# Optimization experiments

Hardware: AMD Instinct MI355X
Metric: run time of the kernel (lower is better)

## Reference

```python
import jax, jax.numpy as jnp
import numpy as np

N = 50000        # nodes
E = 800000       # edges (before self-loops)
IN = 128         # in_dim
H = 2            # heads
C1 = 64          # hidden_dim (per head)
D1 = H * C1      # conv1 concat output = 128
OUT = 64         # out_dim
C2 = 2 * OUT     # conv2 per-head channels = 128 (concat=False -> mean over heads)
NEG = 0.2        # GATv2 leaky_relu negative slope
EPS = 1e-5       # BatchNorm eps


def setup_inputs() -> dict:
    key = jax.random.key(0)
    ks = jax.random.split(key, 14)
    s = 0.05
    inp = {
        "x": jax.random.normal(ks[0], (N, IN), jnp.float32),
        "edge_index": jax.random.randint(ks[1], (2, E), 0, N, dtype=jnp.int32),
        # conv1 (GATv2: lin_l for source, lin_r for target, att vector per head)
        "W_l1": jax.random.normal(ks[2], (IN, D1), jnp.float32) * s,
        "b_l1": jnp.zeros((D1,), jnp.float32),
        "W_r1": jax.random.normal(ks[3], (IN, D1), jnp.float32) * s,
        "b_r1": jnp.zeros((D1,), jnp.float32),
        "att1": jax.random.normal(ks[4], (H, C1), jnp.float32) * s,
        "bias1": jnp.zeros((D1,), jnp.float32),
        # batch_norm1 (affine)
        "gamma1": jnp.ones((D1,), jnp.float32),
        "beta1": jnp.zeros((D1,), jnp.float32),
        # conv2
        "W_l2": jax.random.normal(ks[5], (D1, H * C2), jnp.float32) * s,
        "b_l2": jnp.zeros((H * C2,), jnp.float32),
        "W_r2": jax.random.normal(ks[6], (D1, H * C2), jnp.float32) * s,
        "b_r2": jnp.zeros((H * C2,), jnp.float32),
        "att2": jax.random.normal(ks[7], (H, C2), jnp.float32) * s,
        "bias2": jnp.zeros((C2,), jnp.float32),
    }
    return inp


def gatv2_layer(x, src, dst, W_l, b_l, W_r, b_r, att, bias, concat):
    Hh, Cc = att.shape
    x_l = (x @ W_l + b_l).reshape(N, Hh, Cc)   # source transform
    x_r = (x @ W_r + b_r).reshape(N, Hh, Cc)   # target transform
    # per-edge GATv2 score: att . leaky_relu(x_l[j] + x_r[i])
    e = jax.nn.leaky_relu(x_l[src] + x_r[dst], NEG)      # [E', H, C]
    logit = jnp.einsum("ehc,hc->eh", e, att)              # [E', H]
    # segment softmax over incoming edges of each target node
    m = jax.ops.segment_max(logit, dst, num_segments=N)   # [N, H]
    ex = jnp.exp(logit - m[dst])
    den = jax.ops.segment_sum(ex, dst, num_segments=N)    # [N, H]
    alpha = ex / den[dst]                                  # [E', H]
    out = jax.ops.segment_sum(x_l[src] * alpha[:, :, None], dst, num_segments=N)
    out = out.reshape(N, Hh * Cc) if concat else out.mean(axis=1)
    return out + bias


def batchnorm(x, gamma=None, beta=None):
    mu = x.mean(axis=0)
    var = x.var(axis=0)  # biased variance, as used by BN for normalization
    xn = (x - mu) * jax.lax.rsqrt(var + EPS)
    if gamma is not None:
        xn = xn * gamma + beta
    return xn


def reference(x, edge_index, W_l1, b_l1, W_r1, b_r1, att1, bias1, gamma1, beta1,
              W_l2, b_l2, W_r2, b_r2, att2, bias2):
    loops = jnp.arange(N, dtype=edge_index.dtype)
    src = jnp.concatenate([edge_index[0], loops])  # add self-loops (PyG default)
    dst = jnp.concatenate([edge_index[1], loops])
    h = gatv2_layer(x, src, dst, W_l1, b_l1, W_r1, b_r1, att1, bias1, True)
    h = jax.nn.relu(batchnorm(h, gamma1, beta1))
    o = gatv2_layer(h, src, dst, W_l2, b_l2, W_r2, b_r2, att2, bias2, False)
    mu_part = batchnorm(o[:, :OUT])                      # affine=False
    return jnp.concatenate([mu_part, jax.nn.softplus(o[:, OUT:])], axis=1)
```

## Files before the change

### kernel.cpp

```cpp
#include <hip/hip_runtime.h>
#include <hip/hip_bf16.h>
#include <math.h>

#define NNODES 50000
#define NEDGES 800000
#define EPTOT  (NEDGES + NNODES)
#define NEG_SLOPE 0.2f
#define BN_EPS 1e-5f
#define LOG2E 1.44269504088896f
#define ESLOT 64

#define PB_SC  3321
#define PB_W1  (PB_SC + 128)
#define PB_W2  (PB_W1 + 256)

typedef __hip_bfloat16 bf16;
typedef __attribute__((ext_vector_type(8))) short short8;
typedef __attribute__((ext_vector_type(4))) float f32x4;
typedef __attribute__((ext_vector_type(2))) float f32x2;

__device__ __forceinline__ unsigned short f2us(float f){
    return (unsigned short)(__bfloat16_as_ushort(__float2bfloat16(f)));
}
__device__ __forceinline__ f32x2 unpk(unsigned int w){
    union { unsigned int u; float f; } lo, hi;
    lo.u = w << 16; hi.u = w & 0xffff0000u;
    f32x2 r; r.x = lo.f; r.y = hi.f; return r;
}
__device__ __forceinline__ f32x2 pkmax(f32x2 a, f32x2 b){
#if __has_builtin(__builtin_elementwise_max)
    return __builtin_elementwise_max(a, b);
#else
    f32x2 r; r.x = fmaxf(a.x, b.x); r.y = fmaxf(a.y, b.y); return r;
#endif
}
__device__ __forceinline__ unsigned int pack2(float a, float b){
    return (unsigned int)f2us(a) | ((unsigned int)f2us(b) << 16);
}


__global__ __launch_bounds__(256) void misc_prep(
    const int* __restrict__ ei, int* __restrict__ cnt, int* __restrict__ esrc,
    const float* __restrict__ Wl1, const float* __restrict__ Wr1,
    const float* __restrict__ bl1, const float* __restrict__ br1,
    bf16* __restrict__ WT1, float* __restrict__ bc1,
    const float* __restrict__ Wl2, const float* __restrict__ Wr2,
    const float* __restrict__ bl2, const float* __restrict__ br2,
    bf16* __restrict__ WT2, float* __restrict__ bc2)
{
    int b = blockIdx.x;
    if (b < PB_SC){
        int e = b * 256 + threadIdx.x;
        if (e < EPTOT){
            int s, d;
            if (e < NEDGES){ s = ei[e]; d = ei[NEDGES + e]; } else { s = d = e - NEDGES; }
            int pos = atomicAdd(&cnt[d], 1);
            if (pos < ESLOT) esrc[(d << 6) + pos] = s;
        }
    } else if (b < PB_W1){
        int i = (b - PB_SC) * 256 + threadIdx.x;
        int r = i >> 7, k = i & 127;
        const float* W = (r < 128) ? Wl1 : Wr1;
        int c = (r < 128) ? r : r - 128;
        WT1[i] = __float2bfloat16(W[k * 128 + c]);
        if (k == 0) bc1[r] = (r < 128) ? bl1[c] : br1[c];
    } else {
        int i = (b - PB_W1) * 256 + threadIdx.x;
        int r = i >> 7, k = i & 127;
        const float* W = (r < 256) ? Wl2 : Wr2;
        int c = (r < 256) ? r : r - 256;
        WT2[i] = __float2bfloat16(W[k * 256 + c]);
        if (k == 0) bc2[r] = (r < 256) ? bl2[c] : br2[c];
    }
}


template<int DTOT, bool F32A>
__global__ __launch_bounds__(128) void mfma_gemm(
    const void* __restrict__ A, const bf16* __restrict__ WT,
    const float* __restrict__ biascat,
    bf16* __restrict__ xl, bf16* __restrict__ xr)
{
    constexpr int TILES = DTOT / 64;
    int wave = threadIdx.x >> 6;
    int lane = threadIdx.x & 63;
    int quad = lane >> 4;
    int l16  = lane & 15;
    int m0 = blockIdx.x * 128 + wave * 64;
    const short* Ap = (const short*)A;
    const float* Af = (const float*)A;
    const short* Bp = (const short*)WT;

    short8 af[4][4];
    #pragma unroll
    for (int k = 0; k < 4; ++k)
        #pragma unroll
        for (int mt = 0; mt < 4; ++mt){
            int m = m0 + mt * 16 + l16;
            m = (m < NNODES) ? m : (NNODES - 1);
            if (F32A){
                float4 v0 = *(const float4*)(Af + (size_t)m * 128 + k * 32 + quad * 8);
                float4 v1 = *(const float4*)(Af + (size_t)m * 128 + k * 32 + quad * 8 + 4);
                unsigned int* u = (unsigned int*)&af[k][mt];
                u[0] = pack2(v0.x, v0.y); u[1] = pack2(v0.z, v0.w);
                u[2] = pack2(v1.x, v1.y); u[3] = pack2(v1.z, v1.w);
            } else {
                af[k][mt] = *(const short8*)(Ap + (size_t)m * 128 + k * 32 + quad * 8);
            }
        }

    for (int t = 0; t < TILES; ++t){
        int n0 = (blockIdx.y * TILES + t) * 64;
        f32x4 acc[4][4] = {};
        #pragma unroll
        for (int k = 0; k < 4; ++k){
            short8 bfr[4];
            #pragma unroll
            for (int nt = 0; nt < 4; ++nt){
                int n = n0 + nt * 16 + l16;
                bfr[nt] = *(const short8*)(Bp + (size_t)n * 128 + k * 32 + quad * 8);
            }
            #pragma unroll
            for (int mt = 0; mt < 4; ++mt)
                #pragma unroll
                for (int nt = 0; nt < 4; ++nt)
                    acc[mt][nt] = __builtin_amdgcn_mfma_f32_16x16x32_bf16(af[k][mt], bfr[nt], acc[mt][nt], 0, 0, 0);
        }
        #pragma unroll
        for (int nt = 0; nt < 4; ++nt){
            int n = n0 + nt * 16 + l16;
            float bi = biascat[n];
            bf16* outp = (n < DTOT) ? xl : xr;
            int c = (n < DTOT) ? n : n - DTOT;
            #pragma unroll
            for (int mt = 0; mt < 4; ++mt)
                #pragma unroll
                for (int r = 0; r < 4; ++r){
                    int m = m0 + mt * 16 + quad * 4 + r;
                    if (m < NNODES)
                        outp[(size_t)m * DTOT + c] = __float2bfloat16(acc[mt][nt][r] + bi);
                }
        }
    }
}


template<int C, bool MEAN>
__global__ __launch_bounds__(128) void gat_aggregate(
    const bf16* __restrict__ xl, const bf16* __restrict__ xr,
    const float* __restrict__ att, const int* __restrict__ cnt,
    const int* __restrict__ esrc, void* __restrict__ outv,
    const float* __restrict__ bias2)
{
    constexpr int G  = C / 8;
    constexpr int E  = 64 / G;
    constexpr int HC = 2 * C;
    __shared__ float tmp[HC];
    int n    = blockIdx.x;
    int lane = threadIdx.x & 63;
    int head = threadIdx.x >> 6;
    int g    = lane / G;
    int cl   = lane % G;
    int rowoff = head * (C * 2) + cl * 16;
    const char* xlb = (const char*)xl;

    uint4 xw = *(const uint4*)((const char*)xr + (size_t)n * (HC * 2) + rowoff);
    f32x2 xr0 = unpk(xw.x), xr1 = unpk(xw.y), xr2v = unpk(xw.z), xr3 = unpk(xw.w);
    const float* ap = att + head * C + cl * 8;
    f32x2 av0 = {ap[0] * LOG2E, ap[1] * LOG2E};
    f32x2 av1 = {ap[2] * LOG2E, ap[3] * LOG2E};
    f32x2 av2 = {ap[4] * LOG2E, ap[5] * LOG2E};
    f32x2 av3 = {ap[6] * LOG2E, ap[7] * LOG2E};

    int e0 = n << 6;
    int e1 = e0 + cnt[n];

    float den = 0.f;
    f32x2 a0 = {0.f,0.f}, a1 = {0.f,0.f}, a2 = {0.f,0.f}, a3 = {0.f,0.f};
    for (int p0 = e0; p0 < e1; p0 += 2 * E){
        int pa = p0 + g;
        int pb = p0 + E + g;
        float mka = (pa < e1) ? 0.f : -1e30f;
        float mkb = (pb < e1) ? 0.f : -1e30f;
        int sa = esrc[(pa < e1) ? pa : (e1 - 1)];
        int sb = esrc[(pb < e1) ? pb : (e1 - 1)];
        uint4 wa = *(const uint4*)(xlb + (size_t)sa * (HC * 2) + rowoff);
        uint4 wb = *(const uint4*)(xlb + (size_t)sb * (HC * 2) + rowoff);

        f32x2 xa0 = unpk(wa.x), xa1 = unpk(wa.y), xa2 = unpk(wa.z), xa3 = unpk(wa.w);
        f32x2 xb0 = unpk(wb.x), xb1 = unpk(wb.y), xb2 = unpk(wb.z), xb3 = unpk(wb.w);

        f32x2 ua0 = xa0 + xr0, ua1 = xa1 + xr1, ua2 = xa2 + xr2v, ua3 = xa3 + xr3;
        f32x2 ub0 = xb0 + xr0, ub1 = xb1 + xr1, ub2 = xb2 + xr2v, ub3 = xb3 + xr3;

        f32x2 ppa = pkmax(ua0, ua0 * NEG_SLOPE) * av0;
        ppa += pkmax(ua1, ua1 * NEG_SLOPE) * av1;
        ppa += pkmax(ua2, ua2 * NEG_SLOPE) * av2;
        ppa += pkmax(ua3, ua3 * NEG_SLOPE) * av3;
        f32x2 ppb = pkmax(ub0, ub0 * NEG_SLOPE) * av0;
        ppb += pkmax(ub1, ub1 * NEG_SLOPE) * av1;
        ppb += pkmax(ub2, ub2 * NEG_SLOPE) * av2;
        ppb += pkmax(ub3, ub3 * NEG_SLOPE) * av3;
        float parta = ppa.x + ppa.y;
        float partb = ppb.x + ppb.y;
        #pragma unroll
        for (int mask = G / 2; mask >= 1; mask >>= 1){
            parta += __shfl_xor(parta, mask, 64);
            partb += __shfl_xor(partb, mask, 64);
        }
        float exa = exp2f(parta + mka);
        float exb = exp2f(partb + mkb);
        den += exa + exb;
        f32x2 ea = {exa, exa}, eb = {exb, exb};
        a0 += ea * xa0; a1 += ea * xa1; a2 += ea * xa2; a3 += ea * xa3;
        a0 += eb * xb0; a1 += eb * xb1; a2 += eb * xb2; a3 += eb * xb3;
    }

    #pragma unroll
    for (int mask = G; mask < 64; mask <<= 1){
        den  += __shfl_xor(den, mask, 64);
        a0.x += __shfl_xor(a0.x, mask, 64); a0.y += __shfl_xor(a0.y, mask, 64);
        a1.x += __shfl_xor(a1.x, mask, 64); a1.y += __shfl_xor(a1.y, mask, 64);
        a2.x += __shfl_xor(a2.x, mask, 64); a2.y += __shfl_xor(a2.y, mask, 64);
        a3.x += __shfl_xor(a3.x, mask, 64); a3.y += __shfl_xor(a3.y, mask, 64);
    }
    float inv = 1.f / den;

    if (!MEAN){
        if (g == 0){
            uint4 o;
            o.x = pack2(a0.x * inv, a0.y * inv);
            o.y = pack2(a1.x * inv, a1.y * inv);
            o.z = pack2(a2.x * inv, a2.y * inv);
            o.w = pack2(a3.x * inv, a3.y * inv);
            *(uint4*)((char*)outv + (size_t)n * (HC * 2) + rowoff) = o;
        }
    } else {
        if (g == 0){
            float* tp = tmp + head * C + cl * 8;
            tp[0] = a0.x * inv; tp[1] = a0.y * inv;
            tp[2] = a1.x * inv; tp[3] = a1.y * inv;
            tp[4] = a2.x * inv; tp[5] = a2.y * inv;
            tp[6] = a3.x * inv; tp[7] = a3.y * inv;
        }
        __syncthreads();
        if (head == 0 && g == 0){
            float* outp = (float*)outv + (size_t)n * C;
            #pragma unroll
            for (int v = 0; v < 8; ++v){
                int c = cl * 8 + v;
                outp[c] = 0.5f * (tmp[c] + tmp[C + c]) + bias2[c];
            }
        }
    }
}


__global__ void bn_stats_bf16(const unsigned int* __restrict__ x, float* __restrict__ sums){
    __shared__ float ls[1024];
    int t = threadIdx.x;
    int c2 = t & 63;
    int rg = t >> 6;
    float s0 = 0.f, q0 = 0.f, s1 = 0.f, q1 = 0.f;
    for (int r = blockIdx.x * 4 + rg; r < NNODES; r += gridDim.x * 4){
        f32x2 v = unpk(x[(size_t)r * 64 + c2]);
        s0 += v.x; q0 += v.x * v.x;
        s1 += v.y; q1 += v.y * v.y;
    }
    ls[t] = s0; ls[256 + t] = q0; ls[512 + t] = s1; ls[768 + t] = q1;
    __syncthreads();
    if (rg == 0){
        for (int g = 1; g < 4; ++g){
            s0 += ls[g * 64 + c2];       q0 += ls[256 + g * 64 + c2];
            s1 += ls[512 + g * 64 + c2]; q1 += ls[768 + g * 64 + c2];
        }
        atomicAdd(&sums[2 * c2], s0);
        atomicAdd(&sums[128 + 2 * c2], q0);
        atomicAdd(&sums[2 * c2 + 1], s1);
        atomicAdd(&sums[128 + 2 * c2 + 1], q1);
    }
}

__global__ void bn_stats_o2(const float* __restrict__ x, float* __restrict__ sums){
    __shared__ float ls[512];
    int t = threadIdx.x;
    int col = t & 63;
    int rg  = t >> 6;
    float s = 0.f, q = 0.f;
    for (int r = blockIdx.x * 4 + rg; r < NNODES; r += gridDim.x * 4){
        float v = x[(size_t)r * 128 + col];
        s += v; q += v * v;
    }
    ls[t] = s; ls[256 + t] = q;
    __syncthreads();
    if (rg == 0){
        for (int g = 1; g < 4; ++g){ s += ls[g * 64 + col]; q += ls[256 + g * 64 + col]; }
        atomicAdd(&sums[col], s);
        atomicAdd(&sums[64 + col], q);
    }
}

__global__ void bn_apply_relu(const unsigned int* __restrict__ o1, const float* __restrict__ sums,
                              const float* __restrict__ gamma, const float* __restrict__ beta,
                              unsigned int* __restrict__ h){
    int i = blockIdx.x * blockDim.x + threadIdx.x;
    if (i >= NNODES * 64) return;
    int c2 = i & 63;
    int c0 = 2 * c2, c1 = c0 + 1;
    const float inv_n = 1.f / (float)NNODES;
    float mu0 = sums[c0] * inv_n;
    float sc0 = gamma[c0] * rsqrtf(sums[128 + c0] * inv_n - mu0 * mu0 + BN_EPS);
    float sh0 = beta[c0] - mu0 * sc0;
    float mu1 = sums[c1] * inv_n;
    float sc1 = gamma[c1] * rsqrtf(sums[128 + c1] * inv_n - mu1 * mu1 + BN_EPS);
    float sh1 = beta[c1] - mu1 * sc1;
    f32x2 v = unpk(o1[i]);
    float v0 = v.x * sc0 + sh0;
    float v1 = v.y * sc1 + sh1;
    h[i] = pack2(v0 > 0.f ? v0 : 0.f, v1 > 0.f ? v1 : 0.f);
}

__global__ void final_out(const float* __restrict__ o2, const float* __restrict__ sums,
                          float* __restrict__ out){
    int i = blockIdx.x * blockDim.x + threadIdx.x;
    if (i >= NNODES * 128) return;
    int c = i & 127;
    float v = o2[i];
    float r;
    if (c < 64){
        const float inv_n = 1.f / (float)NNODES;
        float mu = sums[c] * inv_n;
        float rsig = rsqrtf(sums[64 + c] * inv_n - mu * mu + BN_EPS);
        r = (v - mu) * rsig;
    } else {
        r = (v > 20.f) ? v : log1pf(__expf(v));
    }
    out[i] = r;
}


extern "C" void kernel_launch(void* const* d_in, const int* in_sizes, int n_in,
                              void* d_out, int out_size, void* d_ws, size_t ws_size,
                              hipStream_t stream) {
    const float* x     = (const float*)d_in[0];
    const int*   ei    = (const int*)d_in[1];
    const float* W_l1  = (const float*)d_in[2];
    const float* b_l1  = (const float*)d_in[3];
    const float* W_r1  = (const float*)d_in[4];
    const float* b_r1  = (const float*)d_in[5];
    const float* att1  = (const float*)d_in[6];
    const float* gamma1 = (const float*)d_in[8];
    const float* beta1  = (const float*)d_in[9];
    const float* W_l2  = (const float*)d_in[10];
    const float* b_l2  = (const float*)d_in[11];
    const float* W_r2  = (const float*)d_in[12];
    const float* b_r2  = (const float*)d_in[13];
    const float* att2  = (const float*)d_in[14];
    const float* bias2 = (const float*)d_in[15];
    float* out = (float*)d_out;

    char* w = (char*)d_ws;
    size_t off = 0;
    auto alloc = [&](size_t bytes) -> void* {
        void* p = w + off;
        off += (bytes + 255) & ~(size_t)255;
        return p;
    };
    const size_t NF  = (size_t)NNODES * 128 * 4;
    bf16*  xl1   = (bf16*) alloc(NF / 2);
    bf16*  xr1   = (bf16*) alloc(NF / 2);
    bf16*  xl2   = (bf16*) alloc(NF);
    bf16*  xr2   = (bf16*) alloc(NF);
    bf16*  hbuf  = (bf16*) alloc(NF / 2);
    unsigned int* o1 = (unsigned int*)alloc(NF / 2);
    float* o2    = (float*)alloc(NF);
    bf16*  WT1   = (bf16*) alloc(256 * 128 * 2);
    bf16*  WT2   = (bf16*) alloc(512 * 128 * 2);
    float* bc1   = (float*)alloc(256 * 4);
    float* bc2   = (float*)alloc(512 * 4);
    int*   cnt    = (int*)  alloc((size_t)NNODES * 4);
    int*   esrc   = (int*)  alloc((size_t)NNODES * ESLOT * 4);
    float* bnsums = (float*)alloc(384 * 4);
    float* bn1s = bnsums;
    float* bn2s = bnsums + 256;

    hipMemsetAsync(cnt, 0, (size_t)NNODES * 4, stream);
    hipMemsetAsync(bnsums, 0, 384 * 4, stream);

    misc_prep<<<PB_W2, 256, 0, stream>>>(ei, cnt, esrc,
                                         W_l1, W_r1, b_l1, b_r1, WT1, bc1,
                                         W_l2, W_r2, b_l2, b_r2, WT2, bc2);

    mfma_gemm<128, true><<<dim3(392, 2), 128, 0, stream>>>(x, WT1, bc1, xl1, xr1);
    gat_aggregate<64, false><<<NNODES, 128, 0, stream>>>(xl1, xr1, att1, cnt, esrc, o1, bias2);

    bn_stats_bf16<<<128, 256, 0, stream>>>(o1, bn1s);
    bn_apply_relu<<<(NNODES * 64 + 255) / 256, 256, 0, stream>>>(o1, bn1s, gamma1, beta1, (unsigned int*)hbuf);

    mfma_gemm<256, false><<<dim3(392, 2), 128, 0, stream>>>(hbuf, WT2, bc2, xl2, xr2);
    gat_aggregate<128, true><<<NNODES, 128, 0, stream>>>(xl2, xr2, att2, cnt, esrc, o2, bias2);

    bn_stats_o2<<<128, 256, 0, stream>>>(o2, bn2s);
    final_out<<<(NNODES * 128 + 255) / 256, 256, 0, stream>>>(o2, bn2s, out);
}
```

Before: 444.5 us.

## Preload edge sources per wave, split GEMM2 across more blocks, vectorize final output

The aggregation kernel now loads all 64 edge-source slots with one coalesced load per lane and broadcasts them via shuffles, replacing per-edge global index loads. The main loop drops masking for the first half of each step and handles the remainder in a separate tail. The second GEMM is split into more column tiles across the grid, the BN stats kernels get more blocks, and final_out processes four floats per thread with vector loads and stores. The edge count is clamped to ESLOT, which silently drops edges for nodes whose in-degree exceeds 64.

```diff
diff --git a/kernel.cpp b/kernel.cpp
--- a/kernel.cpp
+++ b/kernel.cpp
@@ -75,13 +75,12 @@
 }
 
 
-template<int DTOT, bool F32A>
+template<int DTOT, bool F32A, int NT>
 __global__ __launch_bounds__(128) void mfma_gemm(
     const void* __restrict__ A, const bf16* __restrict__ WT,
     const float* __restrict__ biascat,
     bf16* __restrict__ xl, bf16* __restrict__ xr)
 {
-    constexpr int TILES = DTOT / 64;
     int wave = threadIdx.x >> 6;
     int lane = threadIdx.x & 63;
     int quad = lane >> 4;
@@ -109,8 +108,8 @@
             }
         }
 
-    for (int t = 0; t < TILES; ++t){
-        int n0 = (blockIdx.y * TILES + t) * 64;
+    for (int t = 0; t < NT; ++t){
+        int n0 = (blockIdx.y * NT + t) * 64;
         f32x4 acc[4][4] = {};
         #pragma unroll
         for (int k = 0; k < 4; ++k){
@@ -162,9 +161,12 @@
     int g    = lane / G;
     int cl   = lane % G;
     int rowoff = head * (C * 2) + cl * 16;
-    const char* xlb = (const char*)xl;
-
-    uint4 xw = *(const uint4*)((const char*)xr + (size_t)n * (HC * 2) + rowoff);
+    const char* xlp = (const char*)xl;
+
+    int srcAll = esrc[(n << 6) + lane];
+    int cc = cnt[n];
+    int c = (cc < ESLOT) ? cc : ESLOT;
+    uint4 xw = *(const uint4*)((const char*)xr + (unsigned)(n * (HC * 2) + rowoff));
     f32x2 xr0 = unpk(xw.x), xr1 = unpk(xw.y), xr2v = unpk(xw.z), xr3 = unpk(xw.w);
     const float* ap = att + head * C + cl * 8;
     f32x2 av0 = {ap[0] * LOG2E, ap[1] * LOG2E};
@@ -172,20 +174,17 @@
     f32x2 av2 = {ap[4] * LOG2E, ap[5] * LOG2E};
     f32x2 av3 = {ap[6] * LOG2E, ap[7] * LOG2E};
 
-    int e0 = n << 6;
-    int e1 = e0 + cnt[n];
-
     float den = 0.f;
     f32x2 a0 = {0.f,0.f}, a1 = {0.f,0.f}, a2 = {0.f,0.f}, a3 = {0.f,0.f};
-    for (int p0 = e0; p0 < e1; p0 += 2 * E){
-        int pa = p0 + g;
-        int pb = p0 + E + g;
-        float mka = (pa < e1) ? 0.f : -1e30f;
-        float mkb = (pb < e1) ? 0.f : -1e30f;
-        int sa = esrc[(pa < e1) ? pa : (e1 - 1)];
-        int sb = esrc[(pb < e1) ? pb : (e1 - 1)];
-        uint4 wa = *(const uint4*)(xlb + (size_t)sa * (HC * 2) + rowoff);
-        uint4 wb = *(const uint4*)(xlb + (size_t)sb * (HC * 2) + rowoff);
+
+    int p = 0;
+    for (; p + E < c; p += 2 * E){
+        int ib = p + E + g;
+        int sa = __shfl(srcAll, p + g, 64);
+        int sb = __shfl(srcAll, (ib < c) ? ib : (c - 1), 64);
+        float mkb = (ib < c) ? 0.f : -1e30f;
+        uint4 wa = *(const uint4*)(xlp + ((unsigned)sa * (unsigned)(HC * 2) + rowoff));
+        uint4 wb = *(const uint4*)(xlp + ((unsigned)sb * (unsigned)(HC * 2) + rowoff));
 
         f32x2 xa0 = unpk(wa.x), xa1 = unpk(wa.y), xa2 = unpk(wa.z), xa3 = unpk(wa.w);
         f32x2 xb0 = unpk(wb.x), xb1 = unpk(wb.y), xb2 = unpk(wb.z), xb3 = unpk(wb.w);
@@ -208,12 +207,34 @@
             parta += __shfl_xor(parta, mask, 64);
             partb += __shfl_xor(partb, mask, 64);
         }
-        float exa = exp2f(parta + mka);
+        float exa = exp2f(parta);
         float exb = exp2f(partb + mkb);
         den += exa + exb;
         f32x2 ea = {exa, exa}, eb = {exb, exb};
         a0 += ea * xa0; a1 += ea * xa1; a2 += ea * xa2; a3 += ea * xa3;
         a0 += eb * xb0; a1 += eb * xb1; a2 += eb * xb2; a3 += eb * xb3;
+    }
+    if (p < c){
+        int ia = p + g;
+        int sa = __shfl(srcAll, (ia < c) ? ia : (c - 1), 64);
+        float mka = (ia < c) ? 0.f : -1e30f;
+        uint4 wa = *(const uint4*)(xlp + ((unsigned)sa * (unsigned)(HC * 2) + rowoff));
+
+        f32x2 xa0 = unpk(wa.x), xa1 = unpk(wa.y), xa2 = unpk(wa.z), xa3 = unpk(wa.w);
+        f32x2 ua0 = xa0 + xr0, ua1 = xa1 + xr1, ua2 = xa2 + xr2v, ua3 = xa3 + xr3;
+
+        f32x2 ppa = pkmax(ua0, ua0 * NEG_SLOPE) * av0;
+        ppa += pkmax(ua1, ua1 * NEG_SLOPE) * av1;
+        ppa += pkmax(ua2, ua2 * NEG_SLOPE) * av2;
+        ppa += pkmax(ua3, ua3 * NEG_SLOPE) * av3;
+        float parta = ppa.x + ppa.y;
+        #pragma unroll
+        for (int mask = G / 2; mask >= 1; mask >>= 1)
+            parta += __shfl_xor(parta, mask, 64);
+        float exa = exp2f(parta + mka);
+        den += exa;
+        f32x2 ea = {exa, exa};
+        a0 += ea * xa0; a1 += ea * xa1; a2 += ea * xa2; a3 += ea * xa3;
     }
 
     #pragma unroll
@@ -248,8 +269,8 @@
             float* outp = (float*)outv + (size_t)n * C;
             #pragma unroll
             for (int v = 0; v < 8; ++v){
-                int c = cl * 8 + v;
-                outp[c] = 0.5f * (tmp[c] + tmp[C + c]) + bias2[c];
+                int c2 = cl * 8 + v;
+                outp[c2] = 0.5f * (tmp[c2] + tmp[C + c2]) + bias2[c2];
             }
         }
     }
@@ -323,19 +344,28 @@
 __global__ void final_out(const float* __restrict__ o2, const float* __restrict__ sums,
                           float* __restrict__ out){
     int i = blockIdx.x * blockDim.x + threadIdx.x;
-    if (i >= NNODES * 128) return;
-    int c = i & 127;
-    float v = o2[i];
-    float r;
+    if (i >= NNODES * 32) return;
+    float4 v = *(const float4*)(o2 + (size_t)i * 4);
+    int c = (i * 4) & 127;
+    const float* vp = (const float*)&v;
+    float4 r;
+    float* rp = (float*)&r;
     if (c < 64){
         const float inv_n = 1.f / (float)NNODES;
-        float mu = sums[c] * inv_n;
-        float rsig = rsqrtf(sums[64 + c] * inv_n - mu * mu + BN_EPS);
-        r = (v - mu) * rsig;
+        #pragma unroll
+        for (int k = 0; k < 4; ++k){
+            float mu = sums[c + k] * inv_n;
+            float rsig = rsqrtf(sums[64 + c + k] * inv_n - mu * mu + BN_EPS);
+            rp[k] = (vp[k] - mu) * rsig;
+        }
     } else {
-        r = (v > 20.f) ? v : log1pf(__expf(v));
-    }
-    out[i] = r;
+        #pragma unroll
+        for (int k = 0; k < 4; ++k){
+            float x = vp[k];
+            rp[k] = (x > 20.f) ? x : log1pf(__expf(x));
+        }
+    }
+    *(float4*)(out + (size_t)i * 4) = r;
 }
 
 
@@ -391,15 +421,15 @@
                                          W_l1, W_r1, b_l1, b_r1, WT1, bc1,
                                          W_l2, W_r2, b_l2, b_r2, WT2, bc2);
 
-    mfma_gemm<128, true><<<dim3(392, 2), 128, 0, stream>>>(x, WT1, bc1, xl1, xr1);
+    mfma_gemm<128, true, 2><<<dim3(392, 2), 128, 0, stream>>>(x, WT1, bc1, xl1, xr1);
     gat_aggregate<64, false><<<NNODES, 128, 0, stream>>>(xl1, xr1, att1, cnt, esrc, o1, bias2);
 
-    bn_stats_bf16<<<128, 256, 0, stream>>>(o1, bn1s);
+    bn_stats_bf16<<<512, 256, 0, stream>>>(o1, bn1s);
     bn_apply_relu<<<(NNODES * 64 + 255) / 256, 256, 0, stream>>>(o1, bn1s, gamma1, beta1, (unsigned int*)hbuf);
 
-    mfma_gemm<256, false><<<dim3(392, 2), 128, 0, stream>>>(hbuf, WT2, bc2, xl2, xr2);
+    mfma_gemm<256, false, 2><<<dim3(392, 4), 128, 0, stream>>>(hbuf, WT2, bc2, xl2, xr2);
     gat_aggregate<128, true><<<NNODES, 128, 0, stream>>>(xl2, xr2, att2, cnt, esrc, o2, bias2);
 
-    bn_stats_o2<<<128, 256, 0, stream>>>(o2, bn2s);
-    final_out<<<(NNODES * 128 + 255) / 256, 256, 0, stream>>>(o2, bn2s, out);
-}
+    bn_stats_o2<<<512, 256, 0, stream>>>(o2, bn2s);
+    final_out<<<(NNODES * 32 + 255) / 256, 256, 0, stream>>>(o2, bn2s, out);
+}
```

Result: faster. 425.3 us (-4.3%).
